# Optimization experiments

Measured on AMD Instinct MI355X. Metric: run time of the kernel, lower is better.

Reference implementation:

```python
import jax, jax.numpy as jnp
import numpy as np

DELTA_VAR = 0.5
DELTA_DIST = 2.0
ALPHA = 1.0
BETA = 1.0
GAMMA = 0.001

N, E, D, H, W = 2, 16, 48, 160, 160
NUM_C = 32


def _safe_norm(x, axis):
    # L2 norm with zero-safe gradient (matches torch.norm 'fro' over the dim)
    d2 = jnp.sum(x * x, axis=axis)
    nz = d2 > 0
    return jnp.sqrt(jnp.where(nz, d2, 1.0)) * nz


def setup_inputs() -> dict:
    key = jax.random.key(0)
    k1, k2 = jax.random.split(key)
    input_ = jax.random.normal(k1, (N, E, D, H, W), dtype=jnp.float32)
    target = jax.random.randint(k2, (N, D, H, W), 0, NUM_C).astype(jnp.int64)
    return {"input_": input_, "target": target, "C": NUM_C}


def _single_loss(emb, labels, C):
    # emb: [E, V] flattened spatial; labels: [V] int in [0, C)
    V = labels.shape[0]
    counts = jax.ops.segment_sum(jnp.ones((V,), emb.dtype), labels, num_segments=C)  # [C]
    sums = jax.ops.segment_sum(emb.T, labels, num_segments=C)                         # [C, E]
    means = sums / counts[:, None]                                                     # [C, E]

    # variance term: per-voxel distance to own cluster mean (equivalent to the
    # one-hot-expanded CxExSPATIAL formulation after the target mask)
    dist = _safe_norm(emb.T - means[labels], axis=1)                                   # [V]
    hinge = jnp.maximum(dist - DELTA_VAR, 0.0) ** 2
    per_cluster = jax.ops.segment_sum(hinge, labels, num_segments=C) / counts          # [C]
    variance_term = jnp.sum(per_cluster) / C

    # distance term: pairwise cluster-mean repulsion
    diff = means[:, None, :] - means[None, :, :]                                       # [C, C, E]
    dmat = _safe_norm(diff, axis=2)                                                    # [C, C]
    repulsion = 2.0 * DELTA_DIST * (1.0 - jnp.eye(C, dtype=emb.dtype))
    hinged = jnp.maximum(repulsion - dmat, 0.0) ** 2
    distance_term = jnp.sum(hinged) / (C * (C - 1))

    # regularizer: mean L2 norm of cluster means
    regularizer_term = jnp.sum(_safe_norm(means, axis=1)) / C

    return ALPHA * variance_term + BETA * distance_term + GAMMA * regularizer_term


def reference(input_, target, C):
    n = input_.shape[0]
    emb = input_.reshape(n, input_.shape[1], -1)  # [N, E, V]
    lab = target.reshape(n, -1).astype(jnp.int32)  # [N, V]
    losses = jax.vmap(lambda e, l: _single_loss(e, l, C))(emb, lab)
    return jnp.sum(losses) / n
```

## Files before the change

kernel.cpp:

```cpp
#include <hip/hip_runtime.h>
#include <math.h>

constexpr int N_  = 2;
constexpr int E_  = 16;
constexpr int C_  = 32;
constexpr int V_  = 48 * 160 * 160;
constexpr int V4_ = V_ / 4;
constexpr int BLK = 256;

constexpr float DELTA_VAR  = 0.5f;
constexpr float DELTA_DIST = 2.0f;
constexpr float GAMMA      = 0.001f;

constexpr int NCOPY     = 8;
constexpr int MUP       = 20;
constexpr int WS_SUMT   = 0;
constexpr int WS_CNT    = WS_SUMT + NCOPY * N_ * E_ * C_;
constexpr int WS_VAR    = WS_CNT  + NCOPY * N_ * C_;
constexpr int WS_TK     = WS_VAR  + NCOPY * N_;
constexpr int WS_MU     = WS_TK + 4;
constexpr int WS_ZERO   = WS_TK + 4;

constexpr int GV = 1024;

using short8 = __attribute__((ext_vector_type(8))) short;
using f32x4  = __attribute__((ext_vector_type(4))) float;

__device__ __forceinline__ unsigned short f2bf(float f) {
    unsigned u = __float_as_uint(f);
    return (unsigned short)((u + 0x7FFFu + ((u >> 16) & 1u)) >> 16);
}
__device__ __forceinline__ unsigned packlab(int4 t) {
    return (unsigned)t.x | ((unsigned)t.y << 8) | ((unsigned)t.z << 16) | ((unsigned)t.w << 24);
}
__device__ __forceinline__ float gload(const float* p) {
    return __hip_atomic_load(p, __ATOMIC_RELAXED, __HIP_MEMORY_SCOPE_AGENT);
}

constexpr int XPAD = 520;
__global__ __launch_bounds__(BLK) void sums_mfma(
    const float4* __restrict__ x4, const int4* __restrict__ t4,
    float* __restrict__ ws)
{
    __shared__ unsigned short s_xb[2][E_ * XPAD];

    const int n     = blockIdx.y;
    const int gtile = blockIdx.x * 2048;
    const int tid   = threadIdx.x;
    const int lane  = tid & 63;
    const int wid   = tid >> 6;
    const int myc   = lane & 15;
    const int quad  = lane >> 4;

    const short one = (short)0x3F80;
    short8 A_ones = {one, one, one, one, one, one, one, one};

    f32x4 acc_lo = {0.f,0.f,0.f,0.f}, acc_hi = {0.f,0.f,0.f,0.f};
    f32x4 cnt_lo = {0.f,0.f,0.f,0.f}, cnt_hi = {0.f,0.f,0.f,0.f};

    float4 R[8];
    {
        const int tb4 = gtile >> 2;
        #pragma unroll
        for (int k = 0; k < 8; ++k) {
            const int i = k * BLK + tid, e = i >> 7, v4 = i & 127;
            R[k] = x4[((size_t)(n * E_ + e)) * V4_ + tb4 + v4];
        }
    }

    #pragma unroll
    for (int t = 0; t < 4; ++t) {
        const int tbase4 = (gtile + t * 512) >> 2;
        unsigned short* buf = s_xb[t & 1];

        #pragma unroll
        for (int k = 0; k < 8; ++k) {
            const int i = k * BLK + tid, e = i >> 7, v4 = i & 127;
            uint2 p;
            p.x = (unsigned)f2bf(R[k].x) | ((unsigned)f2bf(R[k].y) << 16);
            p.y = (unsigned)f2bf(R[k].z) | ((unsigned)f2bf(R[k].w) << 16);
            *(uint2*)&buf[e * XPAD + v4 * 4] = p;
        }
        const int wbase = wid * 128;
        int4 P[4], Q[4];
        #pragma unroll
        for (int s = 0; s < 4; ++s) {
            const int b4 = tbase4 + ((wbase + s * 32 + quad * 8) >> 2);
            P[s] = t4[(size_t)n * V4_ + b4];
            Q[s] = t4[(size_t)n * V4_ + b4 + 1];
        }
        if (t < 3) {
            const int nb4 = (gtile + (t + 1) * 512) >> 2;
            #pragma unroll
            for (int k = 0; k < 8; ++k) {
                const int i = k * BLK + tid, e = i >> 7, v4 = i & 127;
                R[k] = x4[((size_t)(n * E_ + e)) * V4_ + nb4 + v4];
            }
        }

        __builtin_amdgcn_sched_barrier(0);
        asm volatile("s_waitcnt lgkmcnt(0)");
        __builtin_amdgcn_s_barrier();
        __builtin_amdgcn_sched_barrier(0);

        #pragma unroll
        for (int s = 0; s < 4; ++s) {
            const int lvb = wbase + s * 32;
            const short8 A = *(const short8*)&buf[myc * XPAD + lvb + quad * 8];
            const unsigned la = packlab(P[s]), lb2 = packlab(Q[s]);
            short8 Blo, Bhi;
            #pragma unroll
            for (int j = 0; j < 4; ++j) {
                const int c0 = (la  >> (8 * j)) & 255;
                const int c1 = (lb2 >> (8 * j)) & 255;
                Blo[j]     = (c0 == myc)      ? one : (short)0;
                Bhi[j]     = (c0 == myc + 16) ? one : (short)0;
                Blo[4 + j] = (c1 == myc)      ? one : (short)0;
                Bhi[4 + j] = (c1 == myc + 16) ? one : (short)0;
            }
            acc_lo = __builtin_amdgcn_mfma_f32_16x16x32_bf16(A,      Blo, acc_lo, 0, 0, 0);
            acc_hi = __builtin_amdgcn_mfma_f32_16x16x32_bf16(A,      Bhi, acc_hi, 0, 0, 0);
            cnt_lo = __builtin_amdgcn_mfma_f32_16x16x32_bf16(A_ones, Blo, cnt_lo, 0, 0, 0);
            cnt_hi = __builtin_amdgcn_mfma_f32_16x16x32_bf16(A_ones, Bhi, cnt_hi, 0, 0, 0);
        }
    }

    float* s_red = (float*)&s_xb[0][0];
    #pragma unroll
    for (int r = 0; r < 4; ++r) {
        s_red[wid * 512 + lane * 8 + r]     = acc_lo[r];
        s_red[wid * 512 + lane * 8 + 4 + r] = acc_hi[r];
    }
    if (quad == 0) {
        s_red[2048 + wid * 32 + myc]      = cnt_lo[0];
        s_red[2048 + wid * 32 + myc + 16] = cnt_hi[0];
    }
    __syncthreads();

    const int kc = blockIdx.x & (NCOPY - 1);
    float* gsumT = ws + WS_SUMT + kc * (N_ * E_ * C_);
    float* gcntk = ws + WS_CNT  + kc * (N_ * C_);
    #pragma unroll
    for (int u = 0; u < 2; ++u) {
        const int combo = tid * 2 + u;
        const int l = combo >> 3, k = combo & 7;
        const int e = (l >> 4) * 4 + (k & 3);
        const int c = (l & 15) + 16 * (k >> 2);
        const float v = s_red[combo] + s_red[512 + combo]
                      + s_red[1024 + combo] + s_red[1536 + combo];
        unsafeAtomicAdd(&gsumT[(n * E_ + e) * C_ + c], v);
    }
    if (tid < C_) {
        const float v = s_red[2048 + tid] + s_red[2048 + 32 + tid]
                      + s_red[2048 + 64 + tid] + s_red[2048 + 96 + tid];
        unsafeAtomicAdd(&gcntk[n * C_ + tid], v);
    }
}

__global__ __launch_bounds__(BLK) void k_mu(float* __restrict__ ws)
{
    const float* gS = ws + WS_SUMT;
    const float* gC = ws + WS_CNT;
    float*       mu = ws + WS_MU;
    const int tid = threadIdx.x;
    for (int i = tid; i < N_ * C_ * E_; i += BLK) {
        const int n2 = i >> 9;
        const int r  = i & 511;
        const int c  = r >> 4, e = r & 15;
        float s = 0.f, cc = 0.f;
        #pragma unroll
        for (int k = 0; k < NCOPY; ++k) {
            s  += gS[k * (N_ * E_ * C_) + (n2 * E_ + e) * C_ + c];
            cc += gC[k * (N_ * C_) + n2 * C_ + c];
        }
        mu[(n2 * C_ + c) * MUP + e] = s / cc;
        if (e == 0) mu[(n2 * C_ + c) * MUP + 16] = 1.0f / (cc * (float)C_);
    }
}

__global__ __launch_bounds__(BLK, 4) void k_var(
    const float4* __restrict__ x4, const int4* __restrict__ t4,
    float* __restrict__ ws, float* __restrict__ out)
{
    __shared__ float s_mu[N_ * C_ * MUP];
    __shared__ float s_aux[8];
    __shared__ unsigned s_flag;

    float* gvar = ws + WS_VAR;
    const int bid = blockIdx.x, tid = threadIdx.x;
    const int lane = tid & 63, wid = tid >> 6;

    {
        const float* mu = ws + WS_MU;
        for (int i = tid; i < N_ * C_ * MUP; i += BLK) s_mu[i] = mu[i];
    }
    __syncthreads();

    float va0 = 0.f, va1 = 0.f;
    for (int g = bid * BLK + tid; g < N_ * V4_; g += GV * BLK) {
        const int n  = (g >= V4_) ? 1 : 0;
        const int vg = g - n * V4_;
        const int4 t = t4[g];
        const float4* __restrict__ xr = x4 + (size_t)n * E_ * V4_ + vg;
        float4 xs[16];
        #pragma unroll
        for (int e = 0; e < 16; ++e) xs[e] = xr[(size_t)e * V4_];

        const int mb = n * (C_ * MUP);
        const int b0 = mb + t.x * MUP, b1 = mb + t.y * MUP;
        const int b2 = mb + t.z * MUP, b3 = mb + t.w * MUP;
        const float w0 = s_mu[b0 + 16], w1 = s_mu[b1 + 16];
        const float w2 = s_mu[b2 + 16], w3 = s_mu[b3 + 16];

        float d0 = 0.f, d1 = 0.f, d2 = 0.f, d3 = 0.f;
        #pragma unroll
        for (int e = 0; e < 16; ++e) {
            const float mu0 = s_mu[b0 + e];
            const float mu1 = s_mu[b1 + e];
            const float mu2 = s_mu[b2 + e];
            const float mu3 = s_mu[b3 + e];
            d0 += (xs[e].x - mu0) * (xs[e].x - mu0);
            d1 += (xs[e].y - mu1) * (xs[e].y - mu1);
            d2 += (xs[e].z - mu2) * (xs[e].z - mu2);
            d3 += (xs[e].w - mu3) * (xs[e].w - mu3);
        }
        const float h0 = fmaxf(sqrtf(d0) - DELTA_VAR, 0.f);
        const float h1 = fmaxf(sqrtf(d1) - DELTA_VAR, 0.f);
        const float h2 = fmaxf(sqrtf(d2) - DELTA_VAR, 0.f);
        const float h3 = fmaxf(sqrtf(d3) - DELTA_VAR, 0.f);
        const float vv = h0 * h0 * w0 + h1 * h1 * w1 + h2 * h2 * w2 + h3 * h3 * w3;
        va0 += (n == 0) ? vv : 0.f;
        va1 += (n == 0) ? 0.f : vv;
    }

    #pragma unroll
    for (int off = 32; off > 0; off >>= 1) {
        va0 += __shfl_down(va0, off, 64);
        va1 += __shfl_down(va1, off, 64);
    }
    if (lane == 0) { s_aux[wid * 2] = va0; s_aux[wid * 2 + 1] = va1; }
    __syncthreads();
    if (tid == 0) {
        const float t0 = s_aux[0] + s_aux[2] + s_aux[4] + s_aux[6];
        const float t1 = s_aux[1] + s_aux[3] + s_aux[5] + s_aux[7];
        const int kc = bid & (NCOPY - 1);
        unsafeAtomicAdd(&gvar[kc * N_ + 0], t0);
        unsafeAtomicAdd(&gvar[kc * N_ + 1], t1);
        __threadfence();
        unsigned* tk = (unsigned*)(ws + WS_TK);
        s_flag = (atomicAdd(tk, 1u) == (unsigned)(GV - 1)) ? 1u : 0u;
    }
    __syncthreads();

    if (s_flag) {
        __threadfence();
        float local = 0.f;
        if (tid < NCOPY * N_) local += gload(&gvar[tid]);

        for (int n = 0; n < N_; ++n) {
            const float* mu = s_mu + n * (C_ * MUP);
            if (tid < C_) {
                const int c = tid;
                float d2 = 0.f;
                #pragma unroll
                for (int e = 0; e < E_; ++e) {
                    const float m = mu[c * MUP + e];
                    d2 += m * m;
                }
                const float nm = d2 > 0.f ? sqrtf(d2) : 0.f;
                local += GAMMA * nm / (float)C_;
            }
            for (int t2 = tid; t2 < C_ * C_; t2 += BLK) {
                const int i = t2 >> 5, j = t2 & 31;
                if (i != j) {
                    float d2 = 0.f;
                    #pragma unroll
                    for (int e = 0; e < E_; ++e) {
                        const float diff = mu[i * MUP + e] - mu[j * MUP + e];
                        d2 += diff * diff;
                    }
                    const float d = d2 > 0.f ? sqrtf(d2) : 0.f;
                    const float h = fmaxf(2.0f * DELTA_DIST - d, 0.f);
                    local += (h * h) / (float)(C_ * (C_ - 1));
                }
            }
        }

        #pragma unroll
        for (int off = 32; off > 0; off >>= 1)
            local += __shfl_down(local, off, 64);
        if (lane == 0) s_aux[wid] = local;
        __syncthreads();
        if (tid == 0)
            out[0] = (s_aux[0] + s_aux[1] + s_aux[2] + s_aux[3]) / (float)N_;
    }
}

extern "C" void kernel_launch(void* const* d_in, const int* in_sizes, int n_in,
                              void* d_out, int out_size, void* d_ws, size_t ws_size,
                              hipStream_t stream) {
    const float4* x4 = (const float4*)d_in[0];
    const int4*   t4 = (const int4*)d_in[1];
    float* ws  = (float*)d_ws;
    float* out = (float*)d_out;

    hipMemsetAsync(d_ws, 0, WS_ZERO * sizeof(float), stream);

    sums_mfma<<<dim3(600, N_), BLK, 0, stream>>>(x4, t4, ws);
    k_mu     <<<1,             BLK, 0, stream>>>(ws);
    k_var    <<<dim3(GV),      BLK, 0, stream>>>(x4, t4, ws, out);
}
```

Measured before the change: 298.6 us.

## Load MFMA operands directly from global and fold mean computation into last block

The sums kernel no longer stages embeddings through a bf16 LDS tile. Each lane now loads its own channel row straight from global memory, converts it to bf16 in registers, and uses a two-deep software pipeline of loads. The separate single-block k_mu launch is removed: a ticket counter lets the last sums block compute the cluster means. This cuts one kernel launch and the LDS round trip and barriers, but each lane now reads strided rows per channel and the final block does serial extra work.

Measured after the change: 458.2 us. +53.5%, slower.

```diff
diff --git a/kernel.cpp b/kernel.cpp
--- a/kernel.cpp
+++ b/kernel.cpp
@@ -17,11 +17,13 @@
 constexpr int WS_SUMT   = 0;
 constexpr int WS_CNT    = WS_SUMT + NCOPY * N_ * E_ * C_;
 constexpr int WS_VAR    = WS_CNT  + NCOPY * N_ * C_;
-constexpr int WS_TK     = WS_VAR  + NCOPY * N_;
-constexpr int WS_MU     = WS_TK + 4;
-constexpr int WS_ZERO   = WS_TK + 4;
-
-constexpr int GV = 1024;
+constexpr int WS_TK1    = WS_VAR  + NCOPY * N_;
+constexpr int WS_TK2    = WS_TK1 + 1;
+constexpr int WS_MU     = WS_TK1 + 4;
+constexpr int WS_ZERO   = WS_MU;
+
+constexpr int GS_TOT = 600 * N_;
+constexpr int GV     = 1024;
 
 using short8 = __attribute__((ext_vector_type(8))) short;
 using f32x4  = __attribute__((ext_vector_type(4))) float;
@@ -37,12 +39,12 @@
     return __hip_atomic_load(p, __ATOMIC_RELAXED, __HIP_MEMORY_SCOPE_AGENT);
 }
 
-constexpr int XPAD = 520;
 __global__ __launch_bounds__(BLK) void sums_mfma(
     const float4* __restrict__ x4, const int4* __restrict__ t4,
     float* __restrict__ ws)
 {
-    __shared__ unsigned short s_xb[2][E_ * XPAD];
+    __shared__ float s_red[2176];
+    __shared__ unsigned s_flag;
 
     const int n     = blockIdx.y;
     const int gtile = blockIdx.x * 2048;
@@ -58,74 +60,55 @@
     f32x4 acc_lo = {0.f,0.f,0.f,0.f}, acc_hi = {0.f,0.f,0.f,0.f};
     f32x4 cnt_lo = {0.f,0.f,0.f,0.f}, cnt_hi = {0.f,0.f,0.f,0.f};
 
-    float4 R[8];
-    {
-        const int tb4 = gtile >> 2;
-        #pragma unroll
-        for (int k = 0; k < 8; ++k) {
-            const int i = k * BLK + tid, e = i >> 7, v4 = i & 127;
-            R[k] = x4[((size_t)(n * E_ + e)) * V4_ + tb4 + v4];
-        }
-    }
+    const float4* __restrict__ xrow = x4 + (size_t)(n * E_ + myc) * V4_;
+    const int4*   __restrict__ t4n  = t4 + (size_t)n * V4_;
+    const int base4 = (gtile + wid * 512 + quad * 8) >> 2;
+
+#define LOADS(X0, X1, P, Q, s) do {            \
+        X0 = xrow[base4 + (s) * 8];            \
+        X1 = xrow[base4 + (s) * 8 + 1];        \
+        P  = t4n [base4 + (s) * 8];            \
+        Q  = t4n [base4 + (s) * 8 + 1];        \
+    } while (0)
+
+#define STEP(X0, X1, P, Q) do {                                              \
+        short8 A;                                                            \
+        A[0] = (short)f2bf(X0.x); A[1] = (short)f2bf(X0.y);                  \
+        A[2] = (short)f2bf(X0.z); A[3] = (short)f2bf(X0.w);                  \
+        A[4] = (short)f2bf(X1.x); A[5] = (short)f2bf(X1.y);                  \
+        A[6] = (short)f2bf(X1.z); A[7] = (short)f2bf(X1.w);                  \
+        const unsigned la = packlab(P), lb2 = packlab(Q);                    \
+        short8 Blo, Bhi;                                                     \
+        _Pragma("unroll")                                                    \
+        for (int j = 0; j < 4; ++j) {                                        \
+            const int c0 = (la  >> (8 * j)) & 255;                           \
+            const int c1 = (lb2 >> (8 * j)) & 255;                           \
+            Blo[j]     = (c0 == myc)      ? one : (short)0;                  \
+            Bhi[j]     = (c0 == myc + 16) ? one : (short)0;                  \
+            Blo[4 + j] = (c1 == myc)      ? one : (short)0;                  \
+            Bhi[4 + j] = (c1 == myc + 16) ? one : (short)0;                  \
+        }                                                                    \
+        acc_lo = __builtin_amdgcn_mfma_f32_16x16x32_bf16(A,      Blo, acc_lo, 0, 0, 0); \
+        acc_hi = __builtin_amdgcn_mfma_f32_16x16x32_bf16(A,      Bhi, acc_hi, 0, 0, 0); \
+        cnt_lo = __builtin_amdgcn_mfma_f32_16x16x32_bf16(A_ones, Blo, cnt_lo, 0, 0, 0); \
+        cnt_hi = __builtin_amdgcn_mfma_f32_16x16x32_bf16(A_ones, Bhi, cnt_hi, 0, 0, 0); \
+    } while (0)
+
+    float4 X0a, X1a, X0b, X1b;
+    int4   Pa, Qa, Pb, Qb;
+    LOADS(X0a, X1a, Pa, Qa, 0);
+    LOADS(X0b, X1b, Pb, Qb, 1);
 
     #pragma unroll
-    for (int t = 0; t < 4; ++t) {
-        const int tbase4 = (gtile + t * 512) >> 2;
-        unsigned short* buf = s_xb[t & 1];
-
-        #pragma unroll
-        for (int k = 0; k < 8; ++k) {
-            const int i = k * BLK + tid, e = i >> 7, v4 = i & 127;
-            uint2 p;
-            p.x = (unsigned)f2bf(R[k].x) | ((unsigned)f2bf(R[k].y) << 16);
-            p.y = (unsigned)f2bf(R[k].z) | ((unsigned)f2bf(R[k].w) << 16);
-            *(uint2*)&buf[e * XPAD + v4 * 4] = p;
-        }
-        const int wbase = wid * 128;
-        int4 P[4], Q[4];
-        #pragma unroll
-        for (int s = 0; s < 4; ++s) {
-            const int b4 = tbase4 + ((wbase + s * 32 + quad * 8) >> 2);
-            P[s] = t4[(size_t)n * V4_ + b4];
-            Q[s] = t4[(size_t)n * V4_ + b4 + 1];
-        }
-        if (t < 3) {
-            const int nb4 = (gtile + (t + 1) * 512) >> 2;
-            #pragma unroll
-            for (int k = 0; k < 8; ++k) {
-                const int i = k * BLK + tid, e = i >> 7, v4 = i & 127;
-                R[k] = x4[((size_t)(n * E_ + e)) * V4_ + nb4 + v4];
-            }
-        }
-
-        __builtin_amdgcn_sched_barrier(0);
-        asm volatile("s_waitcnt lgkmcnt(0)");
-        __builtin_amdgcn_s_barrier();
-        __builtin_amdgcn_sched_barrier(0);
-
-        #pragma unroll
-        for (int s = 0; s < 4; ++s) {
-            const int lvb = wbase + s * 32;
-            const short8 A = *(const short8*)&buf[myc * XPAD + lvb + quad * 8];
-            const unsigned la = packlab(P[s]), lb2 = packlab(Q[s]);
-            short8 Blo, Bhi;
-            #pragma unroll
-            for (int j = 0; j < 4; ++j) {
-                const int c0 = (la  >> (8 * j)) & 255;
-                const int c1 = (lb2 >> (8 * j)) & 255;
-                Blo[j]     = (c0 == myc)      ? one : (short)0;
-                Bhi[j]     = (c0 == myc + 16) ? one : (short)0;
-                Blo[4 + j] = (c1 == myc)      ? one : (short)0;
-                Bhi[4 + j] = (c1 == myc + 16) ? one : (short)0;
-            }
-            acc_lo = __builtin_amdgcn_mfma_f32_16x16x32_bf16(A,      Blo, acc_lo, 0, 0, 0);
-            acc_hi = __builtin_amdgcn_mfma_f32_16x16x32_bf16(A,      Bhi, acc_hi, 0, 0, 0);
-            cnt_lo = __builtin_amdgcn_mfma_f32_16x16x32_bf16(A_ones, Blo, cnt_lo, 0, 0, 0);
-            cnt_hi = __builtin_amdgcn_mfma_f32_16x16x32_bf16(A_ones, Bhi, cnt_hi, 0, 0, 0);
-        }
-    }
-
-    float* s_red = (float*)&s_xb[0][0];
+    for (int s = 0; s < 16; s += 2) {
+        STEP(X0a, X1a, Pa, Qa);
+        if (s + 2 < 16) LOADS(X0a, X1a, Pa, Qa, s + 2);
+        STEP(X0b, X1b, Pb, Qb);
+        if (s + 3 < 16) LOADS(X0b, X1b, Pb, Qb, s + 3);
+    }
+#undef LOADS
+#undef STEP
+
     #pragma unroll
     for (int r = 0; r < 4; ++r) {
         s_red[wid * 512 + lane * 8 + r]     = acc_lo[r];
@@ -155,26 +138,32 @@
                       + s_red[2048 + 64 + tid] + s_red[2048 + 96 + tid];
         unsafeAtomicAdd(&gcntk[n * C_ + tid], v);
     }
-}
-
-__global__ __launch_bounds__(BLK) void k_mu(float* __restrict__ ws)
-{
-    const float* gS = ws + WS_SUMT;
-    const float* gC = ws + WS_CNT;
-    float*       mu = ws + WS_MU;
-    const int tid = threadIdx.x;
-    for (int i = tid; i < N_ * C_ * E_; i += BLK) {
-        const int n2 = i >> 9;
-        const int r  = i & 511;
-        const int c  = r >> 4, e = r & 15;
-        float s = 0.f, cc = 0.f;
-        #pragma unroll
-        for (int k = 0; k < NCOPY; ++k) {
-            s  += gS[k * (N_ * E_ * C_) + (n2 * E_ + e) * C_ + c];
-            cc += gC[k * (N_ * C_) + n2 * C_ + c];
+
+    __threadfence();
+    __syncthreads();
+    if (tid == 0) {
+        unsigned* tk = (unsigned*)(ws + WS_TK1);
+        s_flag = (atomicAdd(tk, 1u) == (unsigned)(GS_TOT - 1)) ? 1u : 0u;
+    }
+    __syncthreads();
+    if (s_flag) {
+        __threadfence();
+        const float* gS = ws + WS_SUMT;
+        const float* gC = ws + WS_CNT;
+        float*       mu = ws + WS_MU;
+        for (int i = tid; i < N_ * C_ * E_; i += BLK) {
+            const int n2 = i >> 9;
+            const int r  = i & 511;
+            const int c  = r >> 4, e = r & 15;
+            float s = 0.f, cc = 0.f;
+            #pragma unroll
+            for (int k = 0; k < NCOPY; ++k) {
+                s  += gload(&gS[k * (N_ * E_ * C_) + (n2 * E_ + e) * C_ + c]);
+                cc += gload(&gC[k * (N_ * C_) + n2 * C_ + c]);
+            }
+            mu[(n2 * C_ + c) * MUP + e] = s / cc;
+            if (e == 0) mu[(n2 * C_ + c) * MUP + 16] = 1.0f / (cc * (float)C_);
         }
-        mu[(n2 * C_ + c) * MUP + e] = s / cc;
-        if (e == 0) mu[(n2 * C_ + c) * MUP + 16] = 1.0f / (cc * (float)C_);
     }
 }
 
@@ -247,7 +236,7 @@
         unsafeAtomicAdd(&gvar[kc * N_ + 0], t0);
         unsafeAtomicAdd(&gvar[kc * N_ + 1], t1);
         __threadfence();
-        unsigned* tk = (unsigned*)(ws + WS_TK);
+        unsigned* tk = (unsigned*)(ws + WS_TK2);
         s_flag = (atomicAdd(tk, 1u) == (unsigned)(GV - 1)) ? 1u : 0u;
     }
     __syncthreads();
@@ -307,6 +296,5 @@
     hipMemsetAsync(d_ws, 0, WS_ZERO * sizeof(float), stream);
 
     sums_mfma<<<dim3(600, N_), BLK, 0, stream>>>(x4, t4, ws);
-    k_mu     <<<1,             BLK, 0, stream>>>(ws);
     k_var    <<<dim3(GV),      BLK, 0, stream>>>(x4, t4, ws, out);
 }
```

## Fold cluster-mean kernel into sums kernel via last-block ticket, retile grid

Applied to the files above, without the earlier changes.

Removes the separate single-block k_mu launch. The last sums_mfma block, found with an atomic ticket counter, now computes the cluster means. The sums grid also drops from 600 to 480 blocks per batch, so each block handles 5 tiles instead of 4, which changes per-block work and wave balance across CUs. The change saves one kernel launch gap, at the cost of a serialized tail in the final block and an extra fence and barrier in every block.

After: 416.4 us. 1.39x slower.

```diff
diff --git a/kernel.cpp b/kernel.cpp
--- a/kernel.cpp
+++ b/kernel.cpp
@@ -17,11 +17,16 @@
 constexpr int WS_SUMT   = 0;
 constexpr int WS_CNT    = WS_SUMT + NCOPY * N_ * E_ * C_;
 constexpr int WS_VAR    = WS_CNT  + NCOPY * N_ * C_;
-constexpr int WS_TK     = WS_VAR  + NCOPY * N_;
-constexpr int WS_MU     = WS_TK + 4;
-constexpr int WS_ZERO   = WS_TK + 4;
-
-constexpr int GV = 1024;
+constexpr int WS_TK1    = WS_VAR  + NCOPY * N_;
+constexpr int WS_TK2    = WS_TK1 + 1;
+constexpr int WS_MU     = WS_TK1 + 4;
+constexpr int WS_ZERO   = WS_MU;
+
+constexpr int SB_PB  = 480;
+constexpr int VPB_   = V_ / SB_PB;
+constexpr int NT_    = VPB_ / 512;
+constexpr int GS_TOT = SB_PB * N_;
+constexpr int GV     = 1024;
 
 using short8 = __attribute__((ext_vector_type(8))) short;
 using f32x4  = __attribute__((ext_vector_type(4))) float;
@@ -43,9 +48,10 @@
     float* __restrict__ ws)
 {
     __shared__ unsigned short s_xb[2][E_ * XPAD];
+    __shared__ unsigned s_flag;
 
     const int n     = blockIdx.y;
-    const int gtile = blockIdx.x * 2048;
+    const int gtile = blockIdx.x * VPB_;
     const int tid   = threadIdx.x;
     const int lane  = tid & 63;
     const int wid   = tid >> 6;
@@ -69,7 +75,7 @@
     }
 
     #pragma unroll
-    for (int t = 0; t < 4; ++t) {
+    for (int t = 0; t < NT_; ++t) {
         const int tbase4 = (gtile + t * 512) >> 2;
         unsigned short* buf = s_xb[t & 1];
 
@@ -89,7 +95,7 @@
             P[s] = t4[(size_t)n * V4_ + b4];
             Q[s] = t4[(size_t)n * V4_ + b4 + 1];
         }
-        if (t < 3) {
+        if (t + 1 < NT_) {
             const int nb4 = (gtile + (t + 1) * 512) >> 2;
             #pragma unroll
             for (int k = 0; k < 8; ++k) {
@@ -125,6 +131,7 @@
         }
     }
 
+    __syncthreads();
     float* s_red = (float*)&s_xb[0][0];
     #pragma unroll
     for (int r = 0; r < 4; ++r) {
@@ -155,26 +162,32 @@
                       + s_red[2048 + 64 + tid] + s_red[2048 + 96 + tid];
         unsafeAtomicAdd(&gcntk[n * C_ + tid], v);
     }
-}
-
-__global__ __launch_bounds__(BLK) void k_mu(float* __restrict__ ws)
-{
-    const float* gS = ws + WS_SUMT;
-    const float* gC = ws + WS_CNT;
-    float*       mu = ws + WS_MU;
-    const int tid = threadIdx.x;
-    for (int i = tid; i < N_ * C_ * E_; i += BLK) {
-        const int n2 = i >> 9;
-        const int r  = i & 511;
-        const int c  = r >> 4, e = r & 15;
-        float s = 0.f, cc = 0.f;
-        #pragma unroll
-        for (int k = 0; k < NCOPY; ++k) {
-            s  += gS[k * (N_ * E_ * C_) + (n2 * E_ + e) * C_ + c];
-            cc += gC[k * (N_ * C_) + n2 * C_ + c];
-        }
-        mu[(n2 * C_ + c) * MUP + e] = s / cc;
-        if (e == 0) mu[(n2 * C_ + c) * MUP + 16] = 1.0f / (cc * (float)C_);
+
+    __threadfence();
+    __syncthreads();
+    if (tid == 0) {
+        unsigned* tk = (unsigned*)(ws + WS_TK1);
+        s_flag = (atomicAdd(tk, 1u) == (unsigned)(GS_TOT - 1)) ? 1u : 0u;
+    }
+    __syncthreads();
+    if (s_flag) {
+        __threadfence();
+        const float* gS = ws + WS_SUMT;
+        const float* gC = ws + WS_CNT;
+        float*       mu = ws + WS_MU;
+        for (int i = tid; i < N_ * C_ * E_; i += BLK) {
+            const int n2 = i >> 9;
+            const int r  = i & 511;
+            const int c  = r >> 4, e = r & 15;
+            float s = 0.f, cc = 0.f;
+            #pragma unroll
+            for (int k = 0; k < NCOPY; ++k) {
+                s  += gload(&gS[k * (N_ * E_ * C_) + (n2 * E_ + e) * C_ + c]);
+                cc += gload(&gC[k * (N_ * C_) + n2 * C_ + c]);
+            }
+            mu[(n2 * C_ + c) * MUP + e] = s / cc;
+            if (e == 0) mu[(n2 * C_ + c) * MUP + 16] = 1.0f / (cc * (float)C_);
+        }
     }
 }
 
@@ -247,7 +260,7 @@
         unsafeAtomicAdd(&gvar[kc * N_ + 0], t0);
         unsafeAtomicAdd(&gvar[kc * N_ + 1], t1);
         __threadfence();
-        unsigned* tk = (unsigned*)(ws + WS_TK);
+        unsigned* tk = (unsigned*)(ws + WS_TK2);
         s_flag = (atomicAdd(tk, 1u) == (unsigned)(GV - 1)) ? 1u : 0u;
     }
     __syncthreads();
@@ -306,7 +319,6 @@
 
     hipMemsetAsync(d_ws, 0, WS_ZERO * sizeof(float), stream);
 
-    sums_mfma<<<dim3(600, N_), BLK, 0, stream>>>(x4, t4, ws);
-    k_mu     <<<1,             BLK, 0, stream>>>(ws);
-    k_var    <<<dim3(GV),      BLK, 0, stream>>>(x4, t4, ws, out);
-}
+    sums_mfma<<<dim3(SB_PB, N_), BLK, 0, stream>>>(x4, t4, ws);
+    k_var    <<<dim3(GV),        BLK, 0, stream>>>(x4, t4, ws, out);
+}
```

## Replace last-block ticket finalization with separate finalize kernel, reorder label loads

Applied to the files above, without the earlier changes.

Removes the atomic ticket counter and thread fences from the variance kernel and moves the distance/regularizer finalization into a separate single-block kernel launched afterward. In the MFMA sums kernel, the label loads are moved after the prefetch of the next embedding tile, and the tile loop is no longer forced to unroll. This removes per-block fence and atomic serialization at the cost of an extra kernel launch, and changes the instruction schedule and register pressure of the sums kernel.

Result: faster. 288.7 us (-3.3%).

```diff
diff --git a/kernel.cpp b/kernel.cpp
--- a/kernel.cpp
+++ b/kernel.cpp
@@ -17,9 +17,8 @@
 constexpr int WS_SUMT   = 0;
 constexpr int WS_CNT    = WS_SUMT + NCOPY * N_ * E_ * C_;
 constexpr int WS_VAR    = WS_CNT  + NCOPY * N_ * C_;
-constexpr int WS_TK     = WS_VAR  + NCOPY * N_;
-constexpr int WS_MU     = WS_TK + 4;
-constexpr int WS_ZERO   = WS_TK + 4;
+constexpr int WS_MU     = WS_VAR  + NCOPY * N_ + 4;
+constexpr int WS_ZERO   = WS_VAR  + NCOPY * N_;
 
 constexpr int GV = 1024;
 
@@ -32,9 +31,6 @@
 }
 __device__ __forceinline__ unsigned packlab(int4 t) {
     return (unsigned)t.x | ((unsigned)t.y << 8) | ((unsigned)t.z << 16) | ((unsigned)t.w << 24);
-}
-__device__ __forceinline__ float gload(const float* p) {
-    return __hip_atomic_load(p, __ATOMIC_RELAXED, __HIP_MEMORY_SCOPE_AGENT);
 }
 
 constexpr int XPAD = 520;
@@ -68,7 +64,6 @@
         }
     }
 
-    #pragma unroll
     for (int t = 0; t < 4; ++t) {
         const int tbase4 = (gtile + t * 512) >> 2;
         unsigned short* buf = s_xb[t & 1];
@@ -80,14 +75,6 @@
             p.x = (unsigned)f2bf(R[k].x) | ((unsigned)f2bf(R[k].y) << 16);
             p.y = (unsigned)f2bf(R[k].z) | ((unsigned)f2bf(R[k].w) << 16);
             *(uint2*)&buf[e * XPAD + v4 * 4] = p;
-        }
-        const int wbase = wid * 128;
-        int4 P[4], Q[4];
-        #pragma unroll
-        for (int s = 0; s < 4; ++s) {
-            const int b4 = tbase4 + ((wbase + s * 32 + quad * 8) >> 2);
-            P[s] = t4[(size_t)n * V4_ + b4];
-            Q[s] = t4[(size_t)n * V4_ + b4 + 1];
         }
         if (t < 3) {
             const int nb4 = (gtile + (t + 1) * 512) >> 2;
@@ -96,6 +83,14 @@
                 const int i = k * BLK + tid, e = i >> 7, v4 = i & 127;
                 R[k] = x4[((size_t)(n * E_ + e)) * V4_ + nb4 + v4];
             }
+        }
+        const int wbase = wid * 128;
+        int4 P[4], Q[4];
+        #pragma unroll
+        for (int s = 0; s < 4; ++s) {
+            const int b4 = tbase4 + ((wbase + s * 32 + quad * 8) >> 2);
+            P[s] = t4[(size_t)n * V4_ + b4];
+            Q[s] = t4[(size_t)n * V4_ + b4 + 1];
         }
 
         __builtin_amdgcn_sched_barrier(0);
@@ -180,11 +175,10 @@
 
 __global__ __launch_bounds__(BLK, 4) void k_var(
     const float4* __restrict__ x4, const int4* __restrict__ t4,
-    float* __restrict__ ws, float* __restrict__ out)
+    float* __restrict__ ws)
 {
     __shared__ float s_mu[N_ * C_ * MUP];
     __shared__ float s_aux[8];
-    __shared__ unsigned s_flag;
 
     float* gvar = ws + WS_VAR;
     const int bid = blockIdx.x, tid = threadIdx.x;
@@ -246,54 +240,64 @@
         const int kc = bid & (NCOPY - 1);
         unsafeAtomicAdd(&gvar[kc * N_ + 0], t0);
         unsafeAtomicAdd(&gvar[kc * N_ + 1], t1);
-        __threadfence();
-        unsigned* tk = (unsigned*)(ws + WS_TK);
-        s_flag = (atomicAdd(tk, 1u) == (unsigned)(GV - 1)) ? 1u : 0u;
-    }
-    __syncthreads();
-
-    if (s_flag) {
-        __threadfence();
-        float local = 0.f;
-        if (tid < NCOPY * N_) local += gload(&gvar[tid]);
-
-        for (int n = 0; n < N_; ++n) {
-            const float* mu = s_mu + n * (C_ * MUP);
-            if (tid < C_) {
-                const int c = tid;
+    }
+}
+
+__global__ __launch_bounds__(BLK) void k_fin(
+    const float* __restrict__ ws, float* __restrict__ out)
+{
+    __shared__ float s_mu[N_ * C_ * MUP];
+    __shared__ float s_aux[4];
+
+    const float* gvar = ws + WS_VAR;
+    const int tid = threadIdx.x;
+    const int lane = tid & 63, wid = tid >> 6;
+
+    {
+        const float* mu = ws + WS_MU;
+        for (int i = tid; i < N_ * C_ * MUP; i += BLK) s_mu[i] = mu[i];
+    }
+    __syncthreads();
+
+    float local = 0.f;
+    if (tid < NCOPY * N_) local += gvar[tid];
+
+    for (int n = 0; n < N_; ++n) {
+        const float* mu = s_mu + n * (C_ * MUP);
+        if (tid < C_) {
+            const int c = tid;
+            float d2 = 0.f;
+            #pragma unroll
+            for (int e = 0; e < E_; ++e) {
+                const float m = mu[c * MUP + e];
+                d2 += m * m;
+            }
+            const float nm = d2 > 0.f ? sqrtf(d2) : 0.f;
+            local += GAMMA * nm / (float)C_;
+        }
+        for (int t2 = tid; t2 < C_ * C_; t2 += BLK) {
+            const int i = t2 >> 5, j = t2 & 31;
+            if (i != j) {
                 float d2 = 0.f;
                 #pragma unroll
                 for (int e = 0; e < E_; ++e) {
-                    const float m = mu[c * MUP + e];
-                    d2 += m * m;
+                    const float diff = mu[i * MUP + e] - mu[j * MUP + e];
+                    d2 += diff * diff;
                 }
-                const float nm = d2 > 0.f ? sqrtf(d2) : 0.f;
-                local += GAMMA * nm / (float)C_;
+                const float d = d2 > 0.f ? sqrtf(d2) : 0.f;
+                const float h = fmaxf(2.0f * DELTA_DIST - d, 0.f);
+                local += (h * h) / (float)(C_ * (C_ - 1));
             }
-            for (int t2 = tid; t2 < C_ * C_; t2 += BLK) {
-                const int i = t2 >> 5, j = t2 & 31;
-                if (i != j) {
-                    float d2 = 0.f;
-                    #pragma unroll
-                    for (int e = 0; e < E_; ++e) {
-                        const float diff = mu[i * MUP + e] - mu[j * MUP + e];
-                        d2 += diff * diff;
-                    }
-                    const float d = d2 > 0.f ? sqrtf(d2) : 0.f;
-                    const float h = fmaxf(2.0f * DELTA_DIST - d, 0.f);
-                    local += (h * h) / (float)(C_ * (C_ - 1));
-                }
-            }
-        }
-
-        #pragma unroll
-        for (int off = 32; off > 0; off >>= 1)
-            local += __shfl_down(local, off, 64);
-        if (lane == 0) s_aux[wid] = local;
-        __syncthreads();
-        if (tid == 0)
-            out[0] = (s_aux[0] + s_aux[1] + s_aux[2] + s_aux[3]) / (float)N_;
-    }
+        }
+    }
+
+    #pragma unroll
+    for (int off = 32; off > 0; off >>= 1)
+        local += __shfl_down(local, off, 64);
+    if (lane == 0) s_aux[wid] = local;
+    __syncthreads();
+    if (tid == 0)
+        out[0] = (s_aux[0] + s_aux[1] + s_aux[2] + s_aux[3]) / (float)N_;
 }
 
 extern "C" void kernel_launch(void* const* d_in, const int* in_sizes, int n_in,
@@ -308,5 +312,6 @@
 
     sums_mfma<<<dim3(600, N_), BLK, 0, stream>>>(x4, t4, ws);
     k_mu     <<<1,             BLK, 0, stream>>>(ws);
-    k_var    <<<dim3(GV),      BLK, 0, stream>>>(x4, t4, ws, out);
-}
+    k_var    <<<dim3(GV),      BLK, 0, stream>>>(x4, t4, ws);
+    k_fin    <<<1,             BLK, 0, stream>>>(ws, out);
+}
```
